# Performance work log

Measured on AMD Instinct MI355X. Metric: run time of the kernel, lower is better.

## Reference

```python
import jax, jax.numpy as jnp
from jax import lax
import numpy as np
import math

B, T, D = 4, 4096, 1024
K, H = 128, 8
KH = K // H
KER = 4
M = 4 * D  # mlp hidden


def _ln(x, g, b):
    m = jnp.mean(x, axis=-1, keepdims=True)
    v = jnp.var(x, axis=-1, keepdims=True)
    return (x - m) / jnp.sqrt(v + 1e-5) * g + b


def setup_inputs() -> dict:
    key = jax.random.key(0)
    ks = jax.random.split(key, 20)
    s = lambda i, shape, sc=0.02: jax.random.normal(ks[i], shape, dtype=jnp.float32) * sc
    inp = {}
    inp["x"] = jax.random.normal(ks[0], (B, T, D), dtype=jnp.float32)
    inp["prev_eig"] = jax.random.normal(ks[1], (B, T, 2 * K), dtype=jnp.float32)
    inp["in_proj_w"] = s(2, (2 * K, D))
    inp["conv_w"] = s(3, (2 * K, 1, KER), 0.3)          # depthwise Conv1d weight
    inp["conv_b"] = s(4, (2 * K,), 0.02)
    inp["mem_gate"] = jnp.float32(-3.0)
    inp["mem_proj_w"] = jnp.eye(2 * K, dtype=jnp.float32) + s(5, (2 * K, 2 * K), 0.02)
    # log_decay uniform in [center-1, center+0.5], center = -2 + 1.5*(1/5)
    center = -2.0 + 1.5 * (1.0 / 5.0)
    inp["log_decay"] = jax.random.uniform(ks[6], (K,), dtype=jnp.float32, minval=center - 1.0, maxval=center + 0.5)
    inp["frequency"] = jnp.linspace(0.0, 2.0 * math.pi * (1.0 - 1.0 / K), K, dtype=jnp.float32)
    inp["coupling"] = jnp.eye(KH, dtype=jnp.float32)[None] + 0.01 * jax.random.normal(ks[7], (H, KH, KH), dtype=jnp.float32) / math.sqrt(KH)
    inp["out_proj_w"] = s(8, (D, 2 * K))
    inp["gate_w"] = s(9, (D, D))
    inp["gate_b"] = jnp.full((D,), -2.0, dtype=jnp.float32)
    inp["mlp_w1"] = s(10, (M, D))
    inp["mlp_b1"] = jnp.zeros((M,), jnp.float32)
    inp["mlp_w2"] = s(11, (D, M))
    inp["mlp_b2"] = jnp.zeros((D,), jnp.float32)
    inp["n1_g"] = jnp.ones((D,), jnp.float32)
    inp["n1_b"] = jnp.zeros((D,), jnp.float32)
    inp["n2_g"] = jnp.ones((D,), jnp.float32)
    inp["n2_b"] = jnp.zeros((D,), jnp.float32)
    return inp


def reference(x, prev_eig, in_proj_w, conv_w, conv_b, mem_gate, mem_proj_w,
              log_decay, frequency, coupling, out_proj_w, gate_w, gate_b,
              mlp_w1, mlp_b1, mlp_w2, mlp_b2, n1_g, n1_b, n2_g, n2_b):
    Bn, Tn, Dn = x.shape
    xn = _ln(x, n1_g, n1_b)
    beta = xn @ in_proj_w.T                                   # [B,T,2K]
    # depthwise causal conv: torch pad=ker-1 both sides then [:, :, :T] == left-pad ker-1 + valid
    ker = conv_w.shape[-1]
    bp = jnp.pad(beta, ((0, 0), (ker - 1, 0), (0, 0))).transpose(0, 2, 1)  # [B,2K,T+ker-1]
    beta = lax.conv_general_dilated(bp, conv_w, (1,), 'VALID',
                                    feature_group_count=conv_w.shape[0],
                                    dimension_numbers=('NCH', 'OIH', 'NCH'))
    beta = jax.nn.silu(beta.transpose(0, 2, 1) + conv_b)       # [B,T,2K]
    br, bi = jnp.split(beta, 2, axis=-1)                       # [B,T,K] each
    # memory injection (has_memory: layer_idx > 0)
    mg = jax.nn.sigmoid(mem_gate)
    pr, pi = jnp.split(prev_eig @ mem_proj_w.T, 2, axis=-1)
    br = br + mg * pr
    bi = bi + mg * pi
    # eigenstate evolution via zero-padded complex FFT convolution
    mag = jax.nn.sigmoid(log_decay)                            # [K]
    n = jnp.arange(Tn, dtype=x.dtype)
    mag_pow = mag[None, :] ** n[:, None]                       # [T,K]
    phase = n[:, None] * frequency[None, :]
    kern = mag_pow * (jnp.cos(phase) + 1j * jnp.sin(phase))    # complex [T,K]
    beta_c = br + 1j * bi
    Bf = jnp.fft.fft(jnp.pad(beta_c, ((0, 0), (0, Tn), (0, 0))), axis=1)  # [B,2T,K]
    Kf = jnp.fft.fft(jnp.pad(kern, ((0, Tn), (0, 0))), axis=0)            # [2T,K]
    c = jnp.fft.ifft(Bf * Kf[None], axis=1)[:, :Tn]
    cr, ci = c.real.astype(x.dtype), c.imag.astype(x.dtype)
    # per-head coupling, batched over heads
    Hh, Kh = coupling.shape[0], coupling.shape[1]
    cr = jnp.einsum('hjk,bthk->bthj', coupling, cr.reshape(Bn, Tn, Hh, Kh)).reshape(Bn, Tn, Hh * Kh)
    ci = jnp.einsum('hjk,bthk->bthj', coupling, ci.reshape(Bn, Tn, Hh, Kh)).reshape(Bn, Tn, Hh * Kh)
    eig = jnp.concatenate([cr, ci], axis=-1)                   # [B,T,2K]
    h = jax.nn.sigmoid(xn @ gate_w.T + gate_b) * (eig @ out_proj_w.T)
    x1 = x + h
    y = _ln(x1, n2_g, n2_b)
    x2 = x1 + jax.nn.silu(y @ mlp_w1.T + mlp_b1) @ mlp_w2.T + mlp_b2
    return (x2, eig)
```

## Files before the change

kernel.cpp:

```cpp
#include <hip/hip_runtime.h>
#include <hip/hip_bf16.h>
#include <math.h>

#define Bn 4
#define Tn 4096
#define Dn 1024
#define Kn 128
#define TWOK 256
#define Hn 8
#define Mmlp 4096
#define NROW (Bn * Tn)
#define TAPS 16

typedef __attribute__((ext_vector_type(8))) short bf16x8;
typedef __attribute__((ext_vector_type(4))) float floatx4;

__device__ __forceinline__ float sigmoidf_(float x) { return 1.f / (1.f + __expf(-x)); }

#define MC_TOT 3555328
__global__ __launch_bounds__(256) void multicast_kernel(
    const float* __restrict__ s0, __hip_bfloat16* __restrict__ d0,
    const float* __restrict__ s1, __hip_bfloat16* __restrict__ d1,
    const float* __restrict__ s2, __hip_bfloat16* __restrict__ d2,
    const float* __restrict__ s3, __hip_bfloat16* __restrict__ d3,
    const float* __restrict__ s4, __hip_bfloat16* __restrict__ d4,
    const float* __restrict__ s5, __hip_bfloat16* __restrict__ d5,
    const float* __restrict__ s6, __hip_bfloat16* __restrict__ d6) {
    for (int i = blockIdx.x * 256 + threadIdx.x; i < MC_TOT; i += gridDim.x * 256) {
        const float* s; __hip_bfloat16* d; int off;
        if      (i <   65536) { s = s0; d = d0; off = i; }
        else if (i <   81920) { s = s1; d = d1; off = i -   65536; }
        else if (i <  147456) { s = s2; d = d2; off = i -   81920; }
        else if (i <  409600) { s = s3; d = d3; off = i -  147456; }
        else if (i < 1458176) { s = s4; d = d4; off = i -  409600; }
        else if (i < 2506752) { s = s5; d = d5; off = i - 1458176; }
        else                  { s = s6; d = d6; off = i - 2506752; }
        const float4 v = ((const float4*)s)[off];
        d[off * 4 + 0] = __float2bfloat16(v.x);
        d[off * 4 + 1] = __float2bfloat16(v.y);
        d[off * 4 + 2] = __float2bfloat16(v.z);
        d[off * 4 + 3] = __float2bfloat16(v.w);
    }
}

__global__ __launch_bounds__(256) void ln_kernel(const float* __restrict__ x,
                                                 const float* __restrict__ g,
                                                 const float* __restrict__ b,
                                                 __hip_bfloat16* __restrict__ out) {
    const int row = blockIdx.x;
    const float4* xr = (const float4*)(x + (size_t)row * Dn);
    float4 v = xr[threadIdx.x];
    float s = v.x + v.y + v.z + v.w;
    float ss = v.x * v.x + v.y * v.y + v.z * v.z + v.w * v.w;
    for (int off = 32; off; off >>= 1) {
        s += __shfl_down(s, off);
        ss += __shfl_down(ss, off);
    }
    __shared__ float rs[4], rss[4];
    const int wv = threadIdx.x >> 6, ln = threadIdx.x & 63;
    if (ln == 0) { rs[wv] = s; rss[wv] = ss; }
    __syncthreads();
    s = rs[0] + rs[1] + rs[2] + rs[3];
    ss = rss[0] + rss[1] + rss[2] + rss[3];
    const float mean = s * (1.f / Dn);
    const float var = ss * (1.f / Dn) - mean * mean;
    const float inv = rsqrtf(var + 1e-5f);
    const float4 gg = ((const float4*)g)[threadIdx.x];
    const float4 bb = ((const float4*)b)[threadIdx.x];
    __hip_bfloat16* op = out + (size_t)row * Dn + threadIdx.x * 4;
    op[0] = __float2bfloat16((v.x - mean) * inv * gg.x + bb.x);
    op[1] = __float2bfloat16((v.y - mean) * inv * gg.y + bb.y);
    op[2] = __float2bfloat16((v.z - mean) * inv * gg.z + bb.z);
    op[3] = __float2bfloat16((v.w - mean) * inv * gg.w + bb.w);
}

template <int EPI, typename CT>
__global__ __launch_bounds__(256, 4)
void gemm_bf(const ushort* __restrict__ A,
             const ushort* __restrict__ B,
             CT* __restrict__ C,
             int M, int N, int Kd,
             const float* __restrict__ bias) {
    __shared__ ushort As[128 * 32];
    __shared__ ushort Bs[128 * 32];
    const int tid = threadIdx.x;
    const int nbx = gridDim.x;
    const int nblk = nbx * gridDim.y;
    int bid = blockIdx.y * nbx + blockIdx.x;
    if ((nblk & 7) == 0)
        bid = (bid & 7) * (nblk >> 3) + (bid >> 3);
    const int m0 = (bid / nbx) * 128, n0 = (bid % nbx) * 128;
    const int wave = tid >> 6, lane = tid & 63;
    const int wm = wave >> 1, wn = wave & 1;
    const int mlane = lane & 15, quad = lane >> 4;

    floatx4 acc[4][4] = {};

    {
        const ushort* Ap = A + (size_t)m0 * Kd;
        const ushort* Bp = B + (size_t)n0 * Kd;
        for (int k0 = 0; k0 < Kd; k0 += 32) {
#pragma unroll
            for (int q = 0; q < 2; ++q) {
                const int c = q * 256 + tid;
                const int row = c >> 2, kc = (c & 3) * 8;
                __builtin_amdgcn_global_load_lds(
                    (const __attribute__((address_space(1))) void*)(Ap + (size_t)row * Kd + k0 + kc),
                    (__attribute__((address_space(3))) void*)(As + c * 8), 16, 0, 0);
                __builtin_amdgcn_global_load_lds(
                    (const __attribute__((address_space(1))) void*)(Bp + (size_t)row * Kd + k0 + kc),
                    (__attribute__((address_space(3))) void*)(Bs + c * 8), 16, 0, 0);
            }
            __syncthreads();
            bf16x8 af[4], bfr[4];
#pragma unroll
            for (int t = 0; t < 4; ++t) {
                af[t]  = *(const bf16x8*)&As[(wm * 64 + t * 16 + mlane) * 32 + quad * 8];
                bfr[t] = *(const bf16x8*)&Bs[(wn * 64 + t * 16 + mlane) * 32 + quad * 8];
            }
#pragma unroll
            for (int i = 0; i < 4; ++i)
#pragma unroll
                for (int j = 0; j < 4; ++j)
                    acc[i][j] = __builtin_amdgcn_mfma_f32_16x16x32_bf16(af[i], bfr[j], acc[i][j], 0, 0, 0);
            __syncthreads();
        }
    }

    float s_pre = 0.f;
    if constexpr (EPI == 1) s_pre = sigmoidf_(bias[0]);

    const int cbase = n0 + wn * 64 + mlane;
#pragma unroll
    for (int i = 0; i < 4; ++i) {
#pragma unroll
        for (int r = 0; r < 4; ++r) {
            const int row = m0 + wm * 64 + i * 16 + quad * 4 + r;
            const size_t ro = (size_t)row * N;
#pragma unroll
            for (int j = 0; j < 4; ++j) {
                const int col = cbase + j * 16;
                const float a = acc[i][j][r];
                float o;
                if constexpr (EPI == 0) o = a;
                else                    o = s_pre * a;
                if constexpr (__is_same(CT, float)) C[ro + col] = o;
                else                                C[ro + col] = __float2bfloat16(o);
            }
        }
    }
}

template <int EPI, typename CT>
__global__ __launch_bounds__(512, 2)
void gemmP(const ushort* __restrict__ A, const ushort* __restrict__ B,
           CT* __restrict__ C, int N, int Kd,
           const float* __restrict__ bias, const float* __restrict__ aux1,
           const __hip_bfloat16* __restrict__ aux2, int cg) {
    __shared__ ushort As[4 * 8192];
    __shared__ ushort Bs[4 * 8192];
    const int tid = threadIdx.x;
    const int nbx = gridDim.x;
    const int nblk = nbx * gridDim.y;
    const int nrows = nblk / nbx;
    int bid = blockIdx.y * nbx + blockIdx.x;
    int mt, ntile;
    if ((nblk & 7) == 0 && cg > 0 && nbx % cg == 0 && nrows % (8 / cg) == 0) {
        const int xcd = bid & 7, i = bid >> 3;
        const int cPerG = nbx / cg;
        const int rPerG = nrows / (8 / cg);
        const int rg = xcd / cg, cgi = xcd % cg;
        mt = rg * rPerG + i / cPerG;
        ntile = cgi * cPerG + i % cPerG;
    } else {
        mt = bid / nbx; ntile = bid % nbx;
    }
    const int m0 = mt * 256, n0 = ntile * 256;
    const int wave = tid >> 6, lane = tid & 63;
    const int wm = wave >> 2, wn = wave & 3;
    const int mlane = lane & 15, quad = lane >> 4;
    const int oswz = (quad ^ ((mlane >> 1) & 3)) * 8;
    const int NT = Kd >> 5;

    const int cA0 = tid, cA1 = 512 + tid;
    const int rA0 = cA0 >> 2, rA1 = cA1 >> 2;
    const ushort* aSrc0 = A + (size_t)(m0 + rA0) * Kd + (((cA0 & 3) ^ ((rA0 >> 1) & 3)) << 3);
    const ushort* aSrc1 = A + (size_t)(m0 + rA1) * Kd + (((cA1 & 3) ^ ((rA1 >> 1) & 3)) << 3);
    const ushort* bSrc0 = B + (size_t)(n0 + rA0) * Kd + (((cA0 & 3) ^ ((rA0 >> 1) & 3)) << 3);
    const ushort* bSrc1 = B + (size_t)(n0 + rA1) * Kd + (((cA1 & 3) ^ ((rA1 >> 1) & 3)) << 3);

    auto stage = [&](int t) {
        const int s = (t & 3) * 8192;
        const int kk = t << 5;
        __builtin_amdgcn_global_load_lds(
            (const __attribute__((address_space(1))) void*)(aSrc0 + kk),
            (__attribute__((address_space(3))) void*)(As + s + cA0 * 8), 16, 0, 0);
        __builtin_amdgcn_global_load_lds(
            (const __attribute__((address_space(1))) void*)(aSrc1 + kk),
            (__attribute__((address_space(3))) void*)(As + s + cA1 * 8), 16, 0, 0);
        __builtin_amdgcn_global_load_lds(
            (const __attribute__((address_space(1))) void*)(bSrc0 + kk),
            (__attribute__((address_space(3))) void*)(Bs + s + cA0 * 8), 16, 0, 0);
        __builtin_amdgcn_global_load_lds(
            (const __attribute__((address_space(1))) void*)(bSrc1 + kk),
            (__attribute__((address_space(3))) void*)(Bs + s + cA1 * 8), 16, 0, 0);
    };

    floatx4 acc[8][4] = {};
    bf16x8 fa0[8], fb0[4], fa1[8], fb1[4];

    const int arow = wm * 128 + mlane;
    const int brow = wn * 64 + mlane;

#define RDSET(FA, FB, T)                                                     \
    {                                                                        \
        const ushort* lA = As + ((T) & 3) * 8192;                            \
        const ushort* lB = Bs + ((T) & 3) * 8192;                            \
        _Pragma("unroll")                                                    \
        for (int f_ = 0; f_ < 8; ++f_)                                       \
            FA[f_] = *(const bf16x8*)(lA + (arow + f_ * 16) * 32 + oswz);    \
        _Pragma("unroll")                                                    \
        for (int g_ = 0; g_ < 4; ++g_)                                       \
            FB[g_] = *(const bf16x8*)(lB + (brow + g_ * 16) * 32 + oswz);    \
    }

#define MMSET(FA, FB)                                                        \
    __builtin_amdgcn_s_setprio(1);                                           \
    _Pragma("unroll")                                                        \
    for (int f_ = 0; f_ < 8; ++f_) {                                         \
        _Pragma("unroll")                                                    \
        for (int g_ = 0; g_ < 4; ++g_) {                                     \
            acc[f_][g_] = __builtin_amdgcn_mfma_f32_16x16x32_bf16(           \
                FA[f_], FB[g_], acc[f_][g_], 0, 0, 0);                       \
        }                                                                    \
    }                                                                        \
    __builtin_amdgcn_s_setprio(0);

#define VMW(T)                                                               \
    if ((T) + 1 < NT) { asm volatile("s_waitcnt vmcnt(4)" ::: "memory"); }   \
    else              { asm volatile("s_waitcnt vmcnt(0)" ::: "memory"); }

    stage(0); stage(1);
    VMW(0)
    __builtin_amdgcn_s_barrier();
    RDSET(fa0, fb0, 0)
    if (2 < NT) stage(2);
    VMW(1)
    __builtin_amdgcn_s_barrier();
    RDSET(fa1, fb1, 1)
    if (3 < NT) stage(3);
    MMSET(fa0, fb0)
    for (int u = 1; u < (NT >> 1); ++u) {
        const int te = 2 * u;
        VMW(te)
        __builtin_amdgcn_s_barrier();
        RDSET(fa0, fb0, te)
        if (te + 2 < NT) stage(te + 2);
        MMSET(fa1, fb1)
        const int to = te + 1;
        VMW(to)
        __builtin_amdgcn_s_barrier();
        RDSET(fa1, fb1, to)
        if (to + 2 < NT) stage(to + 2);
        MMSET(fa0, fb0)
    }
    MMSET(fa1, fb1)
#undef RDSET
#undef MMSET
#undef VMW

    const int cbase = n0 + wn * 64 + mlane;
#pragma unroll
    for (int f = 0; f < 8; ++f) {
#pragma unroll
        for (int r = 0; r < 4; ++r) {
            const int row = m0 + wm * 128 + f * 16 + quad * 4 + r;
            const size_t ro = (size_t)row * N;
#pragma unroll
            for (int g = 0; g < 4; ++g) {
                const int col = cbase + g * 16;
                const float av = acc[f][g][r];
                float o;
                if constexpr (EPI == 0) {
                    o = av;
                } else if constexpr (EPI == 2) {
                    o = aux1[ro + col] + sigmoidf_(av + bias[col]) * __bfloat162float(aux2[ro + col]);
                } else if constexpr (EPI == 3) {
                    const float tt = av + bias[col];
                    o = tt * sigmoidf_(tt);
                } else {
                    o = av + bias[col] + aux1[ro + col];
                }
                if constexpr (__is_same(CT, float)) C[ro + col] = o;
                else                                C[ro + col] = __float2bfloat16(o);
            }
        }
    }
}

#define TCH 256
#define BROWS (TCH + TAPS + 2)
#define UROWS (TCH + TAPS - 1)

__global__ __launch_bounds__(256) void cfc_kernel(const float* __restrict__ beta,
                                                  const float* __restrict__ mgp,
                                                  const float* __restrict__ conv_w,
                                                  const float* __restrict__ conv_b,
                                                  const float* __restrict__ log_decay,
                                                  const float* __restrict__ freq,
                                                  const float* __restrict__ coup,
                                                  float* __restrict__ eig,
                                                  __hip_bfloat16* __restrict__ eig_bf) {
    const int b = blockIdx.z, h = blockIdx.y, t0 = blockIdx.x * TCH;
    const int tid = threadIdx.x;

    __shared__ float sbeta[BROWS * 32];
    __shared__ float su[UROWS * 33];
    __shared__ float str[16 * TAPS], sti[16 * TAPS];
    __shared__ float scoup[16 * 16];
    __shared__ float scw[32 * 4], scb[32];

    auto chan = [&](int cg) { return (cg < 16) ? (h * 16 + cg) : (128 + h * 16 + cg - 16); };

    for (int idx = tid; idx < BROWS * 32; idx += 256) {
        const int r = idx >> 5, cg = idx & 31;
        const int t = t0 - (TAPS + 2) + r;
        sbeta[idx] = (t >= 0) ? beta[((size_t)b * Tn + t) * TWOK + chan(cg)] : 0.f;
    }
    for (int idx = tid; idx < UROWS * 32; idx += 256) {
        const int r = idx >> 5, cg = idx & 31;
        const int t = t0 - (TAPS - 1) + r;
        su[r * 33 + cg] = (t >= 0) ? mgp[((size_t)b * Tn + t) * TWOK + chan(cg)] : 0.f;
    }
    if (tid < 128) scw[tid] = conv_w[chan(tid >> 2) * 4 + (tid & 3)];
    else if (tid < 160) scb[tid - 128] = conv_b[chan(tid - 128)];
    scoup[tid] = coup[h * 256 + tid];
    {
        const int k = tid >> 4, d = tid & (TAPS - 1);
        const float mag = sigmoidf_(log_decay[h * 16 + k]);
        const float f = freq[h * 16 + k];
        const float p = powf(mag, (float)d);
        str[k * TAPS + d] = p * cosf(d * f);
        sti[k * TAPS + d] = p * sinf(d * f);
    }
    __syncthreads();

    for (int idx = tid; idx < UROWS * 32; idx += 256) {
        const int r = idx >> 5, cg = idx & 31;
        const int rb = r + 3;
        float v = sbeta[(rb - 3) * 32 + cg] * scw[cg * 4 + 0] +
                  sbeta[(rb - 2) * 32 + cg] * scw[cg * 4 + 1] +
                  sbeta[(rb - 1) * 32 + cg] * scw[cg * 4 + 2] +
                  sbeta[(rb - 0) * 32 + cg] * scw[cg * 4 + 3] + scb[cg];
        v = v * sigmoidf_(v);
        su[r * 33 + cg] += v;
    }
    __syncthreads();

    const int ru = tid + (TAPS - 1);
    float orr[16], oii[16];
#pragma unroll
    for (int j = 0; j < 16; ++j) { orr[j] = 0.f; oii[j] = 0.f; }
#pragma unroll 4
    for (int k = 0; k < 16; ++k) {
        float accr = 0.f, acci = 0.f;
#pragma unroll
        for (int d = 0; d < TAPS; ++d) {
            const float ur = su[(ru - d) * 33 + k];
            const float ui = su[(ru - d) * 33 + 16 + k];
            const float lr = str[k * TAPS + d], li = sti[k * TAPS + d];
            accr += lr * ur - li * ui;
            acci += lr * ui + li * ur;
        }
#pragma unroll
        for (int j = 0; j < 16; ++j) {
            orr[j] += scoup[j * 16 + k] * accr;
            oii[j] += scoup[j * 16 + k] * acci;
        }
    }
    const size_t base = ((size_t)b * Tn + t0 + tid) * TWOK + h * 16;
    float4* er = (float4*)(eig + base);
    float4* ei = (float4*)(eig + base + Kn);
#pragma unroll
    for (int q = 0; q < 4; ++q) {
        er[q] = make_float4(orr[4 * q], orr[4 * q + 1], orr[4 * q + 2], orr[4 * q + 3]);
        ei[q] = make_float4(oii[4 * q], oii[4 * q + 1], oii[4 * q + 2], oii[4 * q + 3]);
    }
#pragma unroll
    for (int j = 0; j < 16; ++j) {
        eig_bf[base + j] = __float2bfloat16(orr[j]);
        eig_bf[base + Kn + j] = __float2bfloat16(oii[j]);
    }
}

extern "C" void kernel_launch(void* const* d_in, const int* in_sizes, int n_in,
                              void* d_out, int out_size, void* d_ws, size_t ws_size,
                              hipStream_t stream) {
    const float* x          = (const float*)d_in[0];
    const float* prev_eig   = (const float*)d_in[1];
    const float* in_proj_w  = (const float*)d_in[2];
    const float* conv_w     = (const float*)d_in[3];
    const float* conv_b     = (const float*)d_in[4];
    const float* mem_gate   = (const float*)d_in[5];
    const float* mem_proj_w = (const float*)d_in[6];
    const float* log_decay  = (const float*)d_in[7];
    const float* frequency  = (const float*)d_in[8];
    const float* coupling   = (const float*)d_in[9];
    const float* out_proj_w = (const float*)d_in[10];
    const float* gate_w     = (const float*)d_in[11];
    const float* gate_b     = (const float*)d_in[12];
    const float* mlp_w1     = (const float*)d_in[13];
    const float* mlp_b1     = (const float*)d_in[14];
    const float* mlp_w2     = (const float*)d_in[15];
    const float* mlp_b2     = (const float*)d_in[16];
    const float* n1_g       = (const float*)d_in[17];
    const float* n1_b       = (const float*)d_in[18];
    const float* n2_g       = (const float*)d_in[19];
    const float* n2_b       = (const float*)d_in[20];

    float* out = (float*)d_out;
    float* eig = out + (size_t)NROW * Dn;

    char* wsb = (char*)d_ws;
    const size_t MB = 1 << 20;
    const bool bigws = ws_size >= 252 * MB;

    float* x1    = (float*)(wsb + 0);
    float* beta  = (float*)(wsb + 0);
    float* mgp   = (float*)(wsb + 16 * MB);
    __hip_bfloat16 *h1, *eig_bf, *peig_bf, *xn_bf, *y_bf, *w1_bf, *w2_bf,
                   *gate_bf, *inpj_bf, *outpj_bf, *mempj_bf;
    if (bigws) {
        h1       = (__hip_bfloat16*)(wsb + 64 * MB);
        xn_bf    = (__hip_bfloat16*)(wsb + 192 * MB);
        y_bf     = (__hip_bfloat16*)(wsb + 192 * MB);
        w1_bf    = (__hip_bfloat16*)(wsb + 224 * MB);
        w2_bf    = (__hip_bfloat16*)(wsb + 232 * MB);
        gate_bf  = (__hip_bfloat16*)(wsb + 240 * MB);
        inpj_bf  = (__hip_bfloat16*)(wsb + 242 * MB);
        outpj_bf = (__hip_bfloat16*)(wsb + 242 * MB + 512 * 1024);
        mempj_bf = (__hip_bfloat16*)(wsb + 243 * MB);
        peig_bf  = (__hip_bfloat16*)(wsb + 244 * MB);
        eig_bf   = (__hip_bfloat16*)(wsb + 244 * MB);
    } else {
        h1       = (__hip_bfloat16*)(wsb + 64 * MB);
        eig_bf   = (__hip_bfloat16*)(wsb + 96 * MB);
        peig_bf  = (__hip_bfloat16*)(wsb + 104 * MB);
        xn_bf    = (__hip_bfloat16*)(wsb + 128 * MB);
        y_bf     = (__hip_bfloat16*)(wsb + 160 * MB);
        w1_bf    = (__hip_bfloat16*)(wsb + 192 * MB);
        w2_bf    = (__hip_bfloat16*)(wsb + 200 * MB);
        gate_bf  = (__hip_bfloat16*)(wsb + 208 * MB);
        inpj_bf  = (__hip_bfloat16*)(wsb + 210 * MB);
        outpj_bf = (__hip_bfloat16*)(wsb + 210 * MB + 512 * 1024);
        mempj_bf = (__hip_bfloat16*)(wsb + 211 * MB);
    }

    multicast_kernel<<<dim3(2048), dim3(256), 0, stream>>>(
        in_proj_w,  inpj_bf,
        mem_proj_w, mempj_bf,
        out_proj_w, outpj_bf,
        gate_w,     gate_bf,
        mlp_w1,     w1_bf,
        mlp_w2,     w2_bf,
        prev_eig,   peig_bf);

    ln_kernel<<<dim3(NROW), dim3(256), 0, stream>>>(x, n1_g, n1_b, xn_bf);
    gemm_bf<0, float><<<dim3(2, 128), dim3(256), 0, stream>>>(
        (const ushort*)xn_bf, (const ushort*)inpj_bf, beta, NROW, TWOK, Dn, nullptr);
    gemm_bf<1, float><<<dim3(2, 128), dim3(256), 0, stream>>>(
        (const ushort*)peig_bf, (const ushort*)mempj_bf, mgp, NROW, TWOK, TWOK, mem_gate);
    cfc_kernel<<<dim3(Tn / TCH, Hn, Bn), dim3(256), 0, stream>>>(
        beta, mgp, conv_w, conv_b, log_decay, frequency, coupling, eig, eig_bf);
    gemmP<0, __hip_bfloat16><<<dim3(4, 64), dim3(512), 0, stream>>>(
        (const ushort*)eig_bf, (const ushort*)outpj_bf, h1, Dn, TWOK,
        nullptr, nullptr, nullptr, 1);
    gemmP<2, float><<<dim3(4, 64), dim3(512), 0, stream>>>(
        (const ushort*)xn_bf, (const ushort*)gate_bf, x1, Dn, Dn,
        gate_b, x, h1, 1);
    ln_kernel<<<dim3(NROW), dim3(256), 0, stream>>>(x1, n2_g, n2_b, y_bf);
    if (bigws) {
        gemmP<3, __hip_bfloat16><<<dim3(16, 64), dim3(512), 0, stream>>>(
            (const ushort*)y_bf, (const ushort*)w1_bf, h1, Mmlp, Dn,
            mlp_b1, nullptr, nullptr, 2);
        gemmP<4, float><<<dim3(4, 64), dim3(512), 0, stream>>>(
            (const ushort*)h1, (const ushort*)w2_bf, out, Dn, Mmlp,
            mlp_b2, x1, nullptr, 1);
    } else {
        for (int ck = 0; ck < 2; ++ck) {
            const size_t roff = (size_t)ck * 8192 * Dn;
            gemmP<3, __hip_bfloat16><<<dim3(16, 32), dim3(512), 0, stream>>>(
                (const ushort*)(y_bf + roff), (const ushort*)w1_bf, h1, Mmlp, Dn,
                mlp_b1, nullptr, nullptr, 2);
            gemmP<4, float><<<dim3(8, 32), dim3(512), 0, stream>>>(
                (const ushort*)h1, (const ushort*)w2_bf, out + roff, Dn, Mmlp,
                mlp_b2, x1 + roff, nullptr, 1);
        }
    }
}
```

Measured before the change: 658.8 us.

## Restructure GEMM main loop to stage two k-tiles per barrier

Changes the bf16 MFMA GEMM mainloop from one wait-and-barrier per k-tile to one per pair of k-tiles. The two stage loads are issued together after the fragment reads and MFMA set, and empty asm register fences keep the fragments ordered. This halves the barrier and vmcnt wait count. In exchange the wait is now a full vmcnt(0) drain, which can expose more global load latency. Removing the second barrier also depends on the LDS buffers being safe to overwrite, since a stage may write into a buffer other waves are still reading.

```diff
diff --git a/kernel.cpp b/kernel.cpp
--- a/kernel.cpp
+++ b/kernel.cpp
@@ -16,6 +16,10 @@
 typedef __attribute__((ext_vector_type(4))) float floatx4;
 
 __device__ __forceinline__ float sigmoidf_(float x) { return 1.f / (1.f + __expf(-x)); }
+
+__device__ __forceinline__ void fencereg_(const bf16x8& a) {
+    asm volatile("" :: "v"(a));
+}
 
 #define MC_TOT 3555328
 __global__ __launch_bounds__(256) void multicast_kernel(
@@ -236,38 +240,38 @@
     }                                                                        \
     __builtin_amdgcn_s_setprio(0);
 
-#define VMW(T)                                                               \
-    if ((T) + 1 < NT) { asm volatile("s_waitcnt vmcnt(4)" ::: "memory"); }   \
-    else              { asm volatile("s_waitcnt vmcnt(0)" ::: "memory"); }
+#define FENCE1()                                                             \
+    {                                                                        \
+        _Pragma("unroll")                                                    \
+        for (int f_ = 0; f_ < 8; ++f_) fencereg_(fa1[f_]);                   \
+        _Pragma("unroll")                                                    \
+        for (int g_ = 0; g_ < 4; ++g_) fencereg_(fb1[g_]);                   \
+    }
 
     stage(0); stage(1);
-    VMW(0)
+    asm volatile("s_waitcnt vmcnt(0)" ::: "memory");
     __builtin_amdgcn_s_barrier();
     RDSET(fa0, fb0, 0)
-    if (2 < NT) stage(2);
-    VMW(1)
-    __builtin_amdgcn_s_barrier();
+    if (2 < NT) { stage(2); stage(3); }
     RDSET(fa1, fb1, 1)
-    if (3 < NT) stage(3);
     MMSET(fa0, fb0)
-    for (int u = 1; u < (NT >> 1); ++u) {
-        const int te = 2 * u;
-        VMW(te)
+    FENCE1()
+    const int NP = NT >> 1;
+    for (int p = 1; p < NP; ++p) {
+        const int t0 = 2 * p;
+        asm volatile("s_waitcnt vmcnt(0)" ::: "memory");
         __builtin_amdgcn_s_barrier();
-        RDSET(fa0, fb0, te)
-        if (te + 2 < NT) stage(te + 2);
+        RDSET(fa0, fb0, t0)
         MMSET(fa1, fb1)
-        const int to = te + 1;
-        VMW(to)
-        __builtin_amdgcn_s_barrier();
-        RDSET(fa1, fb1, to)
-        if (to + 2 < NT) stage(to + 2);
+        if (t0 + 2 < NT) { stage(t0 + 2); stage(t0 + 3); }
+        RDSET(fa1, fb1, t0 + 1)
         MMSET(fa0, fb0)
+        FENCE1()
     }
     MMSET(fa1, fb1)
 #undef RDSET
 #undef MMSET
-#undef VMW
+#undef FENCE1
 
     const int cbase = n0 + wn * 64 + mlane;
 #pragma unroll
```

Result: slower. 677.9 us (+2.9%).
